# Performance work log

Hardware: AMD Instinct MI355X
Metric: run time of the kernel (lower is better)

The kernel has to match this reference:

```python
import jax, jax.numpy as jnp
import numpy as np

EPS = 1e-8  # torch.cosine_similarity eps
TEMPERATURE = 1.0


def setup_inputs() -> dict:
    key = jax.random.key(0)
    ks = jax.random.split(key, 12)
    B = 16384
    inp = {
        "user_ids": jax.random.randint(ks[0], (B, 8), 0, 100000),
        "item_ids": jax.random.randint(ks[1], (B, 4), 0, 50000),
        "sample_weight": jax.random.uniform(ks[2], (B,), jnp.float32, 0.01, 1.0),
        "user_table": jax.random.normal(ks[3], (100000, 64), jnp.float32) * 0.05,
        "item_table": jax.random.normal(ks[4], (50000, 64), jnp.float32) * 0.05,
        "uW1": jax.random.normal(ks[5], (512, 256), jnp.float32) * 0.04,
        "ub1": jnp.zeros((256,), jnp.float32),
        "uW2": jax.random.normal(ks[6], (256, 128), jnp.float32) * 0.06,
        "ub2": jnp.zeros((128,), jnp.float32),
        "iW1": jax.random.normal(ks[7], (256, 256), jnp.float32) * 0.06,
        "ib1": jnp.zeros((256,), jnp.float32),
        "iW2": jax.random.normal(ks[8], (256, 128), jnp.float32) * 0.06,
        "ib2": jnp.zeros((128,), jnp.float32),
        "n_neg": 3,
    }
    return inp


def _tower(ids, table, W1, b1, W2, b2):
    # embedding lookup [B, F, D] -> concat -> [B, F*D], then 2-layer relu MLP
    B = ids.shape[0]
    e = table[ids].reshape(B, -1)
    h = jax.nn.relu(e @ W1 + b1)
    return jax.nn.relu(h @ W2 + b2)


def reference(user_ids, item_ids, sample_weight, user_table, item_table,
              uW1, ub1, uW2, ub2, iW1, ib1, iW2, ib2, n_neg):
    u = _tower(user_ids, user_table, uW1, ub1, uW2, ub2)  # [B, 128]
    v = _tower(item_ids, item_table, iW1, ib1, iW2, ib2)  # [B, 128]
    # cosine similarity per row (torch eps clamp on norms)
    un = jnp.maximum(jnp.linalg.norm(u, axis=1), EPS)
    vn = jnp.maximum(jnp.linalg.norm(v, axis=1), EPS)
    y = jnp.sum(u * v, axis=1) / (un * vn)
    # sampling-bias correction
    y = y - jnp.log(sample_weight)
    # vectorized wrap-around in-batch negative gather:
    # scores[i] = [y[i], y[(i+1)%B], ..., y[(i+n_neg)%B]]
    B = y.shape[0]
    idx = (jnp.arange(B)[:, None] + jnp.arange(n_neg + 1)[None, :]) % B
    scores = y[idx] / TEMPERATURE  # [B, 1+n_neg]
    return scores
```

## Files before the change

### kernel.cpp

```cpp
#include <hip/hip_runtime.h>
#include <math.h>

#define CEPS 1e-8f

typedef __attribute__((ext_vector_type(8))) short bf16x8;
typedef __attribute__((ext_vector_type(4))) float f32x4;
typedef __attribute__((ext_vector_type(4))) unsigned int u32x4;
typedef __attribute__((ext_vector_type(2))) unsigned int u32x2;

__device__ __forceinline__ unsigned short f2bf(float f) {
    unsigned u = __builtin_bit_cast(unsigned, f);
    u += 0x7fffu + ((u >> 16) & 1u);
    return (unsigned short)(u >> 16);
}

__global__ __launch_bounds__(256)
void pack_all(const float* __restrict__ uW1, const float* __restrict__ uW2,
              const float* __restrict__ iW1, const float* __restrict__ iW2,
              unsigned short* __restrict__ o1, unsigned short* __restrict__ o2,
              unsigned short* __restrict__ o3, unsigned short* __restrict__ o4)
{
    int g = blockIdx.x * 256 + threadIdx.x;
    const float* src; unsigned short* dst; int N; int base;
    if (g < 16384)      { src = uW1; dst = o1; N = 256; base = 0;     }
    else if (g < 20480) { src = uW2; dst = o2; N = 128; base = 16384; }
    else if (g < 28672) { src = iW1; dst = o3; N = 256; base = 20480; }
    else                { src = iW2; dst = o4; N = 128; base = 28672; }
    int i = g - base;
    int kg = i / N, n = i - kg * N;
    unsigned short tmp[8];
    #pragma unroll
    for (int j = 0; j < 8; ++j)
        tmp[j] = f2bf(src[(kg * 8 + j) * N + n]);
    *reinterpret_cast<bf16x8*>(dst + ((size_t)i << 3)) =
        *reinterpret_cast<bf16x8*>(tmp);
}


template<int F>
__device__ __forceinline__ void stage_emb(const int* __restrict__ ids,
                                          const float* __restrict__ table,
                                          unsigned short* e_s, int row0, int tid)
{
    constexpr int FC = F * 8;
    constexpr int IT = (32 * FC) / 512;
    int idv[IT];
    #pragma unroll
    for (int it = 0; it < IT; ++it) {
        int c = tid + it * 512;
        int r = c / FC, f = (c % FC) >> 3;
        idv[it] = ids[(row0 + r) * F + f];
    }
    #pragma unroll
    for (int it = 0; it < IT; ++it) {
        int c = tid + it * 512;
        int r = c / FC, rem = c % FC;
        const float* src = table + (size_t)idv[it] * 64 + (rem & 7) * 8;
        float4 aa = *reinterpret_cast<const float4*>(src);
        float4 bb = *reinterpret_cast<const float4*>(src + 4);
        u32x4 pk;
        pk.x = f2bf(aa.x) | ((unsigned)f2bf(aa.y) << 16);
        pk.y = f2bf(aa.z) | ((unsigned)f2bf(aa.w) << 16);
        pk.z = f2bf(bb.x) | ((unsigned)f2bf(bb.y) << 16);
        pk.w = f2bf(bb.z) | ((unsigned)f2bf(bb.w) << 16);
        int byte = r * (F * 128) + rem * 16;
        byte ^= (r & 7) << 4;
        *reinterpret_cast<u32x4*>(reinterpret_cast<char*>(e_s) + byte) = pk;
    }
}

template<int KB>
__device__ __forceinline__ bf16x8 loadA(const unsigned short* s, int ks, int ni,
                                        int l15, int l4)
{
    int row = ni * 16 + l15;
    int byte = row * (KB * 2) + ks * 64 + l4 * 16;
    byte ^= (row & 7) << 4;
    return *reinterpret_cast<const bf16x8*>(
               reinterpret_cast<const char*>(s) + byte);
}

template<int K1>
__device__ __forceinline__ void gemm1(
    const unsigned short* e_s, unsigned short* h_s,
    const unsigned short* __restrict__ W1p, const float* __restrict__ b1,
    int l15, int l4, int wl, const bf16x8* w0)
{
    constexpr int NKS = K1 / 32;
    f32x4 acc[4][2];
    #pragma unroll
    for (int mi = 0; mi < 4; ++mi)
        #pragma unroll
        for (int ni = 0; ni < 2; ++ni) acc[mi][ni] = (f32x4){0.f, 0.f, 0.f, 0.f};

    const unsigned short* Wbase = W1p + ((l4 * 256 + wl * 64 + l15) << 3);
    bf16x8 wf[3][4], ef[2][2];
    #pragma unroll
    for (int mi = 0; mi < 4; ++mi) {
        wf[0][mi] = w0[mi];
        wf[1][mi] = *reinterpret_cast<const bf16x8*>(Wbase + 8192 + (mi << 7));
    }
    #pragma unroll
    for (int ni = 0; ni < 2; ++ni) ef[0][ni] = loadA<K1>(e_s, 0, ni, l15, l4);

    #pragma unroll
    for (int ks = 0; ks < NKS; ++ks) {
        if (ks + 2 < NKS) {
            #pragma unroll
            for (int mi = 0; mi < 4; ++mi)
                wf[(ks + 2) % 3][mi] = *reinterpret_cast<const bf16x8*>(
                    Wbase + (ks + 2) * 8192 + (mi << 7));
        }
        if (ks + 1 < NKS) {
            #pragma unroll
            for (int ni = 0; ni < 2; ++ni)
                ef[(ks + 1) & 1][ni] = loadA<K1>(e_s, ks + 1, ni, l15, l4);
        }
        __builtin_amdgcn_s_setprio(1);
        #pragma unroll
        for (int mi = 0; mi < 4; ++mi)
            #pragma unroll
            for (int ni = 0; ni < 2; ++ni)
                acc[mi][ni] = __builtin_amdgcn_mfma_f32_16x16x32_bf16(
                                  wf[ks % 3][mi], ef[ks & 1][ni], acc[mi][ni], 0, 0, 0);
        __builtin_amdgcn_s_setprio(0);
    }
    #pragma unroll
    for (int mi = 0; mi < 4; ++mi) {
        const float4 bb = *reinterpret_cast<const float4*>(
                              &b1[wl * 64 + mi * 16 + l4 * 4]);
        #pragma unroll
        for (int ni = 0; ni < 2; ++ni) {
            float v0 = acc[mi][ni][0] + bb.x; v0 = v0 > 0.f ? v0 : 0.f;
            float v1 = acc[mi][ni][1] + bb.y; v1 = v1 > 0.f ? v1 : 0.f;
            float v2 = acc[mi][ni][2] + bb.z; v2 = v2 > 0.f ? v2 : 0.f;
            float v3 = acc[mi][ni][3] + bb.w; v3 = v3 > 0.f ? v3 : 0.f;
            u32x2 d;
            d.x = f2bf(v0) | ((unsigned)f2bf(v1) << 16);
            d.y = f2bf(v2) | ((unsigned)f2bf(v3) << 16);
            int row = ni * 16 + l15;
            int w0c = wl * 64 + mi * 16 + l4 * 4;
            int byte = (row * 256 + w0c) * 2;
            byte ^= (row & 7) << 4;
            *reinterpret_cast<u32x2*>(reinterpret_cast<char*>(h_s) + byte) = d;
        }
    }
}

__device__ __forceinline__ void gemm2(
    const unsigned short* h_s, const unsigned short* __restrict__ W2p,
    f32x4 (&acc)[2][2], int l15, int l4, int wl, const bf16x8* w0)
{
    #pragma unroll
    for (int mi = 0; mi < 2; ++mi)
        #pragma unroll
        for (int ni = 0; ni < 2; ++ni) acc[mi][ni] = (f32x4){0.f, 0.f, 0.f, 0.f};

    const unsigned short* Wbase = W2p + ((l4 * 128 + wl * 32 + l15) << 3);
    bf16x8 wf[3][2], hf[2][2];
    #pragma unroll
    for (int mi = 0; mi < 2; ++mi) {
        wf[0][mi] = w0[mi];
        wf[1][mi] = *reinterpret_cast<const bf16x8*>(Wbase + 4096 + (mi << 7));
    }
    #pragma unroll
    for (int ni = 0; ni < 2; ++ni) hf[0][ni] = loadA<256>(h_s, 0, ni, l15, l4);

    #pragma unroll
    for (int ks = 0; ks < 8; ++ks) {
        if (ks + 2 < 8) {
            #pragma unroll
            for (int mi = 0; mi < 2; ++mi)
                wf[(ks + 2) % 3][mi] = *reinterpret_cast<const bf16x8*>(
                    Wbase + (ks + 2) * 4096 + (mi << 7));
        }
        if (ks + 1 < 8) {
            #pragma unroll
            for (int ni = 0; ni < 2; ++ni)
                hf[(ks + 1) & 1][ni] = loadA<256>(h_s, ks + 1, ni, l15, l4);
        }
        __builtin_amdgcn_s_setprio(1);
        #pragma unroll
        for (int mi = 0; mi < 2; ++mi)
            #pragma unroll
            for (int ni = 0; ni < 2; ++ni)
                acc[mi][ni] = __builtin_amdgcn_mfma_f32_16x16x32_bf16(
                                  wf[ks % 3][mi], hf[ks & 1][ni], acc[mi][ni], 0, 0, 0);
        __builtin_amdgcn_s_setprio(0);
    }
}

__global__ __launch_bounds__(512, 4)
void fused_sbc(const int* __restrict__ user_ids,  const int* __restrict__ item_ids,
               const float* __restrict__ user_table, const float* __restrict__ item_table,
               const unsigned short* __restrict__ uW1p, const float* __restrict__ ub1,
               const unsigned short* __restrict__ uW2p, const float* __restrict__ ub2,
               const unsigned short* __restrict__ iW1p, const float* __restrict__ ib1,
               const unsigned short* __restrict__ iW2p, const float* __restrict__ ib2,
               const float* __restrict__ sw, float* __restrict__ out,
               int B, int nn1)
{
    __shared__ __align__(16) unsigned short smem[40960];
    unsigned short* e_u = smem;
    unsigned short* e_i = smem + 16384;
    unsigned short* h_u = smem + 24576;
    unsigned short* h_i = smem + 32768;
    float* V_lds = reinterpret_cast<float*>(smem);
    float* red   = reinterpret_cast<float*>(smem + 16384);

    const int tid  = threadIdx.x;
    const int lane = tid & 63;
    const int w    = tid >> 6;
    const int l15  = lane & 15, l4 = lane >> 4;
    const int role = w >> 2;
    const int wl   = w & 3;
    const int row0 = blockIdx.x * 32;

    const unsigned short* W1sel = role ? iW1p : uW1p;
    const unsigned short* W2sel = role ? iW2p : uW2p;

    bf16x8 w0g1[4];
    {
        const unsigned short* base = W1sel + ((l4 * 256 + wl * 64 + l15) << 3);
        #pragma unroll
        for (int mi = 0; mi < 4; ++mi)
            w0g1[mi] = *reinterpret_cast<const bf16x8*>(base + (mi << 7));
    }
    stage_emb<8>(user_ids, user_table, e_u, row0, tid);
    stage_emb<4>(item_ids, item_table, e_i, row0, tid);
    __syncthreads();

    if (role == 0) gemm1<512>(e_u, h_u, uW1p, ub1, l15, l4, wl, w0g1);
    else           gemm1<256>(e_i, h_i, iW1p, ib1, l15, l4, wl, w0g1);
    bf16x8 w0g2[2];
    {
        const unsigned short* base = W2sel + ((l4 * 128 + wl * 32 + l15) << 3);
        w0g2[0] = *reinterpret_cast<const bf16x8*>(base);
        w0g2[1] = *reinterpret_cast<const bf16x8*>(base + 128);
    }
    __syncthreads();

    f32x4 acc2[2][2];
    if (role == 0) gemm2(h_u, uW2p, acc2, l15, l4, wl, w0g2);
    else           gemm2(h_i, iW2p, acc2, l15, l4, wl, w0g2);

    if (role == 1) {
        float pv[2] = {0.f, 0.f};
        #pragma unroll
        for (int mi = 0; mi < 2; ++mi) {
            const int colb = wl * 32 + mi * 16 + l4 * 4;
            const float4 bv = *reinterpret_cast<const float4*>(&ib2[colb]);
            #pragma unroll
            for (int ni = 0; ni < 2; ++ni) {
                int row = ni * 16 + l15;
                float v0 = acc2[mi][ni][0] + bv.x; v0 = v0 > 0.f ? v0 : 0.f;
                float v1 = acc2[mi][ni][1] + bv.y; v1 = v1 > 0.f ? v1 : 0.f;
                float v2 = acc2[mi][ni][2] + bv.z; v2 = v2 > 0.f ? v2 : 0.f;
                float v3 = acc2[mi][ni][3] + bv.w; v3 = v3 > 0.f ? v3 : 0.f;
                float4 vv = {v0, v1, v2, v3};
                *reinterpret_cast<float4*>(&V_lds[row * 132 + colb]) = vv;
                pv[ni] += v0 * v0 + v1 * v1 + v2 * v2 + v3 * v3;
            }
        }
        #pragma unroll
        for (int ni = 0; ni < 2; ++ni) {
            pv[ni] += __shfl_xor(pv[ni], 16);
            pv[ni] += __shfl_xor(pv[ni], 32);
        }
        if (l4 == 0) {
            #pragma unroll
            for (int ni = 0; ni < 2; ++ni)
                red[(wl * 32 + ni * 16 + l15) * 3 + 2] = pv[ni];
        }
    }
    __syncthreads();

    if (role == 0) {
        float pd[2] = {0.f, 0.f}, pu[2] = {0.f, 0.f};
        #pragma unroll
        for (int mi = 0; mi < 2; ++mi) {
            const int colb = wl * 32 + mi * 16 + l4 * 4;
            const float4 bu = *reinterpret_cast<const float4*>(&ub2[colb]);
            #pragma unroll
            for (int ni = 0; ni < 2; ++ni) {
                int row = ni * 16 + l15;
                float u0 = acc2[mi][ni][0] + bu.x; u0 = u0 > 0.f ? u0 : 0.f;
                float u1 = acc2[mi][ni][1] + bu.y; u1 = u1 > 0.f ? u1 : 0.f;
                float u2 = acc2[mi][ni][2] + bu.z; u2 = u2 > 0.f ? u2 : 0.f;
                float u3 = acc2[mi][ni][3] + bu.w; u3 = u3 > 0.f ? u3 : 0.f;
                const float4 vv = *reinterpret_cast<const float4*>(
                                      &V_lds[row * 132 + colb]);
                pd[ni] += u0 * vv.x + u1 * vv.y + u2 * vv.z + u3 * vv.w;
                pu[ni] += u0 * u0 + u1 * u1 + u2 * u2 + u3 * u3;
            }
        }
        #pragma unroll
        for (int ni = 0; ni < 2; ++ni) {
            pd[ni] += __shfl_xor(pd[ni], 16);
            pd[ni] += __shfl_xor(pd[ni], 32);
            pu[ni] += __shfl_xor(pu[ni], 16);
            pu[ni] += __shfl_xor(pu[ni], 32);
        }
        if (l4 == 0) {
            #pragma unroll
            for (int ni = 0; ni < 2; ++ni) {
                red[(wl * 32 + ni * 16 + l15) * 3 + 0] = pd[ni];
                red[(wl * 32 + ni * 16 + l15) * 3 + 1] = pu[ni];
            }
        }
    }
    __syncthreads();

    if (tid < 32) {
        int row = tid;
        float d = 0.f, su = 0.f, sv = 0.f;
        #pragma unroll
        for (int cg = 0; cg < 4; ++cg) {
            d  += red[(cg * 32 + row) * 3 + 0];
            su += red[(cg * 32 + row) * 3 + 1];
            sv += red[(cg * 32 + row) * 3 + 2];
        }
        float un = fmaxf(sqrtf(su), CEPS);
        float vn = fmaxf(sqrtf(sv), CEPS);
        int grow = row0 + row;
        float yv = d / (un * vn) - logf(sw[grow]);
        for (int j = 0; j < nn1; ++j) {
            int idx = grow - j;
            if (idx < 0) idx += B;
            out[idx * nn1 + j] = yv;
        }
    }
}

extern "C" void kernel_launch(void* const* d_in, const int* in_sizes, int n_in,
                              void* d_out, int out_size, void* d_ws, size_t ws_size,
                              hipStream_t stream)
{
    const int*   user_ids   = (const int*)  d_in[0];
    const int*   item_ids   = (const int*)  d_in[1];
    const float* sw         = (const float*)d_in[2];
    const float* user_table = (const float*)d_in[3];
    const float* item_table = (const float*)d_in[4];
    const float* uW1        = (const float*)d_in[5];
    const float* ub1        = (const float*)d_in[6];
    const float* uW2        = (const float*)d_in[7];
    const float* ub2        = (const float*)d_in[8];
    const float* iW1        = (const float*)d_in[9];
    const float* ib1        = (const float*)d_in[10];
    const float* iW2        = (const float*)d_in[11];
    const float* ib2        = (const float*)d_in[12];

    const int B   = in_sizes[2];
    const int nn1 = out_size / B;

    unsigned short* wp   = (unsigned short*)d_ws;
    unsigned short* uW1p = wp;
    unsigned short* uW2p = wp + 131072;
    unsigned short* iW1p = wp + 163840;
    unsigned short* iW2p = wp + 229376;
    float* out = (float*)d_out;

    pack_all<<<128, 256, 0, stream>>>(uW1, uW2, iW1, iW2,
                                      uW1p, uW2p, iW1p, iW2p);
    fused_sbc<<<B / 32, 512, 0, stream>>>(user_ids, item_ids,
                                          user_table, item_table,
                                          uW1p, ub1, uW2p, ub2,
                                          iW1p, ib1, iW2p, ib2,
                                          sw, out, B, nn1);
}
```

Baseline: 28.30 us.

## Fuse weight packing into main kernel with grid-wide atomic barrier

Removes the separate pack_all launch. The first wavefront of every block now converts a slice of the weights to bf16, then all blocks meet at a global atomic-counter barrier before the GEMMs. The counter is reset each call with a hipMemsetAsync. This trades one kernel launch for a grid barrier, which requires all 512 blocks to be resident at once, and it drops the early prefetch of the first weight fragments so the embedding gather can overlap the packing.

After: 97.27 us. 244% more time.

```diff
diff --git a/kernel.cpp b/kernel.cpp
--- a/kernel.cpp
+++ b/kernel.cpp
@@ -12,28 +12,6 @@
     unsigned u = __builtin_bit_cast(unsigned, f);
     u += 0x7fffu + ((u >> 16) & 1u);
     return (unsigned short)(u >> 16);
-}
-
-__global__ __launch_bounds__(256)
-void pack_all(const float* __restrict__ uW1, const float* __restrict__ uW2,
-              const float* __restrict__ iW1, const float* __restrict__ iW2,
-              unsigned short* __restrict__ o1, unsigned short* __restrict__ o2,
-              unsigned short* __restrict__ o3, unsigned short* __restrict__ o4)
-{
-    int g = blockIdx.x * 256 + threadIdx.x;
-    const float* src; unsigned short* dst; int N; int base;
-    if (g < 16384)      { src = uW1; dst = o1; N = 256; base = 0;     }
-    else if (g < 20480) { src = uW2; dst = o2; N = 128; base = 16384; }
-    else if (g < 28672) { src = iW1; dst = o3; N = 256; base = 20480; }
-    else                { src = iW2; dst = o4; N = 128; base = 28672; }
-    int i = g - base;
-    int kg = i / N, n = i - kg * N;
-    unsigned short tmp[8];
-    #pragma unroll
-    for (int j = 0; j < 8; ++j)
-        tmp[j] = f2bf(src[(kg * 8 + j) * N + n]);
-    *reinterpret_cast<bf16x8*>(dst + ((size_t)i << 3)) =
-        *reinterpret_cast<bf16x8*>(tmp);
 }
 
 
@@ -84,7 +62,7 @@
 __device__ __forceinline__ void gemm1(
     const unsigned short* e_s, unsigned short* h_s,
     const unsigned short* __restrict__ W1p, const float* __restrict__ b1,
-    int l15, int l4, int wl, const bf16x8* w0)
+    int l15, int l4, int wl)
 {
     constexpr int NKS = K1 / 32;
     f32x4 acc[4][2];
@@ -97,7 +75,7 @@
     bf16x8 wf[3][4], ef[2][2];
     #pragma unroll
     for (int mi = 0; mi < 4; ++mi) {
-        wf[0][mi] = w0[mi];
+        wf[0][mi] = *reinterpret_cast<const bf16x8*>(Wbase + (mi << 7));
         wf[1][mi] = *reinterpret_cast<const bf16x8*>(Wbase + 8192 + (mi << 7));
     }
     #pragma unroll
@@ -149,7 +127,7 @@
 
 __device__ __forceinline__ void gemm2(
     const unsigned short* h_s, const unsigned short* __restrict__ W2p,
-    f32x4 (&acc)[2][2], int l15, int l4, int wl, const bf16x8* w0)
+    f32x4 (&acc)[2][2], int l15, int l4, int wl)
 {
     #pragma unroll
     for (int mi = 0; mi < 2; ++mi)
@@ -160,7 +138,7 @@
     bf16x8 wf[3][2], hf[2][2];
     #pragma unroll
     for (int mi = 0; mi < 2; ++mi) {
-        wf[0][mi] = w0[mi];
+        wf[0][mi] = *reinterpret_cast<const bf16x8*>(Wbase + (mi << 7));
         wf[1][mi] = *reinterpret_cast<const bf16x8*>(Wbase + 4096 + (mi << 7));
     }
     #pragma unroll
@@ -193,13 +171,19 @@
 __global__ __launch_bounds__(512, 4)
 void fused_sbc(const int* __restrict__ user_ids,  const int* __restrict__ item_ids,
                const float* __restrict__ user_table, const float* __restrict__ item_table,
-               const unsigned short* __restrict__ uW1p, const float* __restrict__ ub1,
-               const unsigned short* __restrict__ uW2p, const float* __restrict__ ub2,
-               const unsigned short* __restrict__ iW1p, const float* __restrict__ ib1,
-               const unsigned short* __restrict__ iW2p, const float* __restrict__ ib2,
-               const float* __restrict__ sw, float* __restrict__ out,
-               int B, int nn1)
-{
+               const float* __restrict__ uW1, const float* __restrict__ ub1,
+               const float* __restrict__ uW2, const float* __restrict__ ub2,
+               const float* __restrict__ iW1, const float* __restrict__ ib1,
+               const float* __restrict__ iW2, const float* __restrict__ ib2,
+               const float* __restrict__ sw,
+               unsigned short* __restrict__ wp, int* __restrict__ counter,
+               float* __restrict__ out, int B, int nn1)
+{
+    unsigned short* uW1p = wp;
+    unsigned short* uW2p = wp + 131072;
+    unsigned short* iW1p = wp + 163840;
+    unsigned short* iW2p = wp + 229376;
+
     __shared__ __align__(16) unsigned short smem[40960];
     unsigned short* e_u = smem;
     unsigned short* e_i = smem + 16384;
@@ -216,33 +200,46 @@
     const int wl   = w & 3;
     const int row0 = blockIdx.x * 32;
 
-    const unsigned short* W1sel = role ? iW1p : uW1p;
-    const unsigned short* W2sel = role ? iW2p : uW2p;
-
-    bf16x8 w0g1[4];
-    {
-        const unsigned short* base = W1sel + ((l4 * 256 + wl * 64 + l15) << 3);
-        #pragma unroll
-        for (int mi = 0; mi < 4; ++mi)
-            w0g1[mi] = *reinterpret_cast<const bf16x8*>(base + (mi << 7));
-    }
+    if (tid < 64) {
+        for (int g = blockIdx.x * 64 + tid; g < 32768; g += gridDim.x * 64) {
+            const float* src; unsigned short* dst; int N; int base;
+            if (g < 16384)      { src = uW1; dst = uW1p; N = 256; base = 0;     }
+            else if (g < 20480) { src = uW2; dst = uW2p; N = 128; base = 16384; }
+            else if (g < 28672) { src = iW1; dst = iW1p; N = 256; base = 20480; }
+            else                { src = iW2; dst = iW2p; N = 128; base = 28672; }
+            int i = g - base;
+            int kg = i / N, n = i - kg * N;
+            unsigned short tmp[8];
+            #pragma unroll
+            for (int j = 0; j < 8; ++j)
+                tmp[j] = f2bf(src[(kg * 8 + j) * N + n]);
+            *reinterpret_cast<bf16x8*>(dst + ((size_t)i << 3)) =
+                *reinterpret_cast<bf16x8*>(tmp);
+        }
+        __threadfence();
+    }
+
     stage_emb<8>(user_ids, user_table, e_u, row0, tid);
     stage_emb<4>(item_ids, item_table, e_i, row0, tid);
     __syncthreads();
 
-    if (role == 0) gemm1<512>(e_u, h_u, uW1p, ub1, l15, l4, wl, w0g1);
-    else           gemm1<256>(e_i, h_i, iW1p, ib1, l15, l4, wl, w0g1);
-    bf16x8 w0g2[2];
-    {
-        const unsigned short* base = W2sel + ((l4 * 128 + wl * 32 + l15) << 3);
-        w0g2[0] = *reinterpret_cast<const bf16x8*>(base);
-        w0g2[1] = *reinterpret_cast<const bf16x8*>(base + 128);
-    }
+    if (tid == 0) {
+        __hip_atomic_fetch_add(counter, 1, __ATOMIC_ACQ_REL,
+                               __HIP_MEMORY_SCOPE_AGENT);
+        while (__hip_atomic_load(counter, __ATOMIC_ACQUIRE,
+                                 __HIP_MEMORY_SCOPE_AGENT) < (int)gridDim.x) {
+            __builtin_amdgcn_s_sleep(2);
+        }
+    }
+    __syncthreads();
+
+    if (role == 0) gemm1<512>(e_u, h_u, uW1p, ub1, l15, l4, wl);
+    else           gemm1<256>(e_i, h_i, iW1p, ib1, l15, l4, wl);
     __syncthreads();
 
     f32x4 acc2[2][2];
-    if (role == 0) gemm2(h_u, uW2p, acc2, l15, l4, wl, w0g2);
-    else           gemm2(h_i, iW2p, acc2, l15, l4, wl, w0g2);
+    if (role == 0) gemm2(h_u, uW2p, acc2, l15, l4, wl);
+    else           gemm2(h_i, iW2p, acc2, l15, l4, wl);
 
     if (role == 1) {
         float pv[2] = {0.f, 0.f};
@@ -353,18 +350,14 @@
     const int B   = in_sizes[2];
     const int nn1 = out_size / B;
 
-    unsigned short* wp   = (unsigned short*)d_ws;
-    unsigned short* uW1p = wp;
-    unsigned short* uW2p = wp + 131072;
-    unsigned short* iW1p = wp + 163840;
-    unsigned short* iW2p = wp + 229376;
+    unsigned short* wp = (unsigned short*)d_ws;
+    int* counter = (int*)(wp + 262144);
     float* out = (float*)d_out;
 
-    pack_all<<<128, 256, 0, stream>>>(uW1, uW2, iW1, iW2,
-                                      uW1p, uW2p, iW1p, iW2p);
+    hipMemsetAsync(counter, 0, sizeof(int), stream);
     fused_sbc<<<B / 32, 512, 0, stream>>>(user_ids, item_ids,
                                           user_table, item_table,
-                                          uW1p, ub1, uW2p, ub2,
-                                          iW1p, ib1, iW2p, ib2,
-                                          sw, out, B, nn1);
-}
+                                          uW1, ub1, uW2, ub2,
+                                          iW1, ib1, iW2, ib2,
+                                          sw, wp, counter, out, B, nn1);
+}
```
